# Kernel optimization log

Measured on AMD Instinct MI355X. Metric: run time of the kernel, lower is better.

Reference implementation:

```python
import jax, jax.numpy as jnp
import numpy as np

H = 5  # hidden size
SEQ = 512
BATCH = 16384


def _lstm_layer(x, Wih, Whh, bih, bhh):
    # x: (B, S, D_in); weights follow PyTorch layout: W (4H, D), gate order i,f,g,o
    B = x.shape[0]
    b = bih + bhh
    xs = jnp.swapaxes(x, 0, 1)  # (S, B, D_in)
    # precompute input projections for all timesteps: (S, B, 4H)
    xproj = jnp.einsum('sbd,gd->sbg', xs, Wih) + b

    def step(carry, xp):
        h, c = carry
        gates = xp + h @ Whh.T  # (B, 4H)
        i, f, g, o = jnp.split(gates, 4, axis=-1)
        i = jax.nn.sigmoid(i)
        f = jax.nn.sigmoid(f)
        g = jnp.tanh(g)
        o = jax.nn.sigmoid(o)
        c = f * c + i * g
        h = o * jnp.tanh(c)
        return (h, c), h

    h0 = jnp.zeros((B, H), dtype=x.dtype)
    c0 = jnp.zeros((B, H), dtype=x.dtype)
    _, hs = jax.lax.scan(step, (h0, c0), xproj)  # hs: (S, B, H)
    return jnp.swapaxes(hs, 0, 1)  # (B, S, H)


def setup_inputs() -> dict:
    key = jax.random.key(0)
    ks = jax.random.split(key, 13)
    s = 1.0 / np.sqrt(H)
    u = lambda k, shp: jax.random.uniform(k, shp, jnp.float32, -s, s)
    return {
        'x': jax.random.normal(ks[0], (BATCH, SEQ, 1), jnp.float32),
        'Wih0': u(ks[1], (4 * H, 1)),
        'Whh0': u(ks[2], (4 * H, H)),
        'bih0': u(ks[3], (4 * H,)),
        'bhh0': u(ks[4], (4 * H,)),
        'Wih1': u(ks[5], (4 * H, H)),
        'Whh1': u(ks[6], (4 * H, H)),
        'bih1': u(ks[7], (4 * H,)),
        'bhh1': u(ks[8], (4 * H,)),
        'W1': jax.random.uniform(ks[9], (512, SEQ * H), jnp.float32, -1 / np.sqrt(SEQ * H), 1 / np.sqrt(SEQ * H)),
        'b1': jax.random.uniform(ks[10], (512,), jnp.float32, -1 / np.sqrt(SEQ * H), 1 / np.sqrt(SEQ * H)),
        'W2': jax.random.uniform(ks[11], (1, 512), jnp.float32, -1 / np.sqrt(512), 1 / np.sqrt(512)),
        'b2': jax.random.uniform(ks[12], (1,), jnp.float32, -1 / np.sqrt(512), 1 / np.sqrt(512)),
    }


def reference(x, Wih0, Whh0, bih0, bhh0, Wih1, Whh1, bih1, bhh1, W1, b1, W2, b2):
    h = _lstm_layer(x, Wih0, Whh0, bih0, bhh0)   # (B, S, 5)
    h = _lstm_layer(h, Wih1, Whh1, bih1, bhh1)   # (B, S, 5)
    h = h.reshape(h.shape[0], -1)                # (B, S*5)
    h = h @ W1.T + b1                            # (B, 512)
    out = h @ W2.T + b2                          # (B, 1)
    return out
```

## Files before the change

kernel.cpp:

```cpp
#include <hip/hip_runtime.h>

#define BATCH 16384
#define SEQ 512

typedef float f4 __attribute__((ext_vector_type(4)));
typedef _Float16 half4 __attribute__((ext_vector_type(4)));

#define SIGS (-1.44269504088896f)
#define TNHS (-2.88539008177793f)

union HB2 { unsigned int u[2]; half4 h; };

__device__ __forceinline__ float bpermf(int addr, float v) {
    return __int_as_float(__builtin_amdgcn_ds_bpermute(addr, __float_as_int(v)));
}
__device__ __forceinline__ unsigned int h16(float v) {
    return (unsigned int)__builtin_bit_cast(unsigned short, (_Float16)v);
}
__device__ __forceinline__ unsigned int lolo(unsigned int a, unsigned int b) {
    return __builtin_amdgcn_perm(b, a, 0x05040100u);
}

__device__ __forceinline__ void act3(const f4& dA, const f4& dD, const f4& dC,
                                     float& c0, float& c4, float& c1,
                                     float& hA, float& h4, float& hC) {
    float A0 = __builtin_amdgcn_exp2f(dA[0]), F0 = __builtin_amdgcn_exp2f(dA[1]);
    float B0 = __builtin_amdgcn_exp2f(dA[2]), O0 = __builtin_amdgcn_exp2f(dA[3]);
    float A1 = __builtin_amdgcn_exp2f(dD[0]), F1 = __builtin_amdgcn_exp2f(dD[1]);
    float B1 = __builtin_amdgcn_exp2f(dD[2]), O1 = __builtin_amdgcn_exp2f(dD[3]);
    float A2 = __builtin_amdgcn_exp2f(dC[0]), F2 = __builtin_amdgcn_exp2f(dC[1]);
    float B2 = __builtin_amdgcn_exp2f(dC[2]), O2 = __builtin_amdgcn_exp2f(dC[3]);

    float t0 = 1.0f + A0, t1 = 1.0f + A1, t2 = 1.0f + A2;
    float ab0 = fmaf(t0, B0, t0), ab1 = fmaf(t1, B1, t1), ab2 = fmaf(t2, B2, t2);
    float D0 = fmaf(ab0, F0, ab0), D1 = fmaf(ab1, F1, ab1), D2 = fmaf(ab2, F2, ab2);
    float p01 = D0 * D1, p12 = D1 * D2, p02 = D0 * D2;
    float r = __builtin_amdgcn_rcpf(p01 * D2);
    float r0 = r * p12, r1 = r * p02, r2 = r * p01;

    float bm0 = 1.0f - B0, bm1 = 1.0f - B1, bm2 = 1.0f - B2;
    float w0 = fmaf(bm0, F0, bm0), w1 = fmaf(bm1, F1, bm1), w2 = fmaf(bm2, F2, bm2);
    c0 = fmaf(ab0 * r0, c0, w0 * r0);
    c4 = fmaf(ab1 * r1, c4, w1 * r1);
    c1 = fmaf(ab2 * r2, c1, w2 * r2);

    float pc0 = fminf(c0 * TNHS, 17.0f);
    float pc1 = fminf(c4 * TNHS, 17.0f);
    float pc2 = fminf(c1 * TNHS, 17.0f);
    float Ce0 = __builtin_amdgcn_exp2f(pc0);
    float Ce1 = __builtin_amdgcn_exp2f(pc1);
    float Ce2 = __builtin_amdgcn_exp2f(pc2);
    float o0 = 1.0f + O0, o1 = 1.0f + O1, o2 = 1.0f + O2;
    float e0 = fmaf(o0, Ce0, o0), e1 = fmaf(o1, Ce1, o1), e2 = fmaf(o2, Ce2, o2);
    float q01 = e0 * e1, q12 = e1 * e2, q02 = e0 * e2;
    float rr = __builtin_amdgcn_rcpf(q01 * e2);
    hA = (1.0f - Ce0) * (rr * q12);
    h4 = (1.0f - Ce1) * (rr * q02);
    hC = (1.0f - Ce2) * (rr * q01);
}

__global__ __launch_bounds__(256) void collapse_kernel(
    const float* __restrict__ W1, const float* __restrict__ b1,
    const float* __restrict__ W2, const float* __restrict__ b2,
    float* __restrict__ ws)
{
    const int kl = threadIdx.x & 15;
    const int ms = threadIdx.x >> 4;
    const int k  = blockIdx.x * 16 + kl;
    const float* w1p = W1 + (size_t)(ms * 32) * 2560 + k;
    const float* w2p = W2 + ms * 32;
    float acc = 0.f;
    #pragma unroll 8
    for (int m = 0; m < 32; ++m) acc = fmaf(w2p[m], w1p[(size_t)m * 2560], acc);
    __shared__ float red[16][17];
    red[ms][kl] = acc;
    __syncthreads();
    if (ms == 0) {
        float s = 0.f;
        #pragma unroll
        for (int r = 0; r < 16; ++r) s += red[r][kl];
        const int t = k / 5, u = k % 5;
        if (u < 4) ws[8 * t + 2 * u] = s;
        else { ws[8*t + 1] = s; ws[8*t + 3] = s; ws[8*t + 5] = s; ws[8*t + 7] = s; }
    }
    if (blockIdx.x == 0) {
        const int t = threadIdx.x;
        float p = fmaf(W2[t], b1[t], W2[t + 256] * b1[t + 256]);
        #pragma unroll
        for (int off = 32; off > 0; off >>= 1) p += __shfl_down(p, off);
        __shared__ float cred[4];
        if ((t & 63) == 0) cred[t >> 6] = p;
        __syncthreads();
        if (t == 0) ws[4096] = cred[0] + cred[1] + cred[2] + cred[3] + b2[0];
    }
}

__global__ __launch_bounds__(64)
__attribute__((amdgpu_waves_per_eu(1, 1)))
void lstm_fused_kernel(
    const float* __restrict__ x,
    const float* __restrict__ Wih0, const float* __restrict__ Whh0,
    const float* __restrict__ bih0, const float* __restrict__ bhh0,
    const float* __restrict__ Wih1, const float* __restrict__ Whh1,
    const float* __restrict__ bih1, const float* __restrict__ bhh1,
    const float* __restrict__ ws, float* __restrict__ out)
{
    const int lane = threadIdx.x;
    const int e15  = lane & 15;
    const int g    = lane >> 4;
    const int e    = blockIdx.x * 16 + e15;
    const float sc[4] = {SIGS, SIGS, TNHS, SIGS};

    HB2 aL0a, aL0b, aL1a, aL1b;
    {
        const int m = e15;
        {
            const int u = m >> 2, gi = m & 3, gr = gi * 5 + u;
            const float s = sc[gi];
            float w0 = Whh0[gr * 5 + g];
            float w1 = (g == 0) ? Wih0[gr] : (g == 1 ? Whh0[gr * 5 + 4] : 0.f);
            aL0a.u[0] = h16(w0 * s) | (h16(w1 * s) << 16);
            aL0a.u[1] = 0u;
        }
        {
            float w0 = 0.f, w1 = 0.f, s = 0.f;
            if (m >= 4 && m < 8) {
                const int gi = m - 4, gr = gi * 5 + 4;
                s = sc[gi];
                w0 = Whh0[gr * 5 + g];
                w1 = (g == 0) ? Wih0[gr] : (g == 1 ? Whh0[gr * 5 + 4] : 0.f);
            }
            aL0b.u[0] = h16(w0 * s) | (h16(w1 * s) << 16);
            aL0b.u[1] = 0u;
        }
        {
            const int u = m >> 2, gi = m & 3, gr = gi * 5 + u;
            const float s = sc[gi];
            float w0 = Wih1[gr * 5 + g];
            float w1 = Whh1[gr * 5 + g];
            float w2 = (g == 1) ? Wih1[gr * 5 + 4] : (g == 2 ? Whh1[gr * 5 + 4] : 0.f);
            aL1a.u[0] = h16(w0 * s) | (h16(w1 * s) << 16);
            aL1a.u[1] = h16(w2 * s);
        }
        {
            float w0 = 0.f, w1 = 0.f, w2 = 0.f, s = 0.f;
            if (m >= 8 && m < 12) {
                const int gi = m - 8, gr = gi * 5 + 4;
                s = sc[gi];
                w0 = Wih1[gr * 5 + g];
                w1 = Whh1[gr * 5 + g];
                w2 = (g == 1) ? Wih1[gr * 5 + 4] : (g == 2 ? Whh1[gr * 5 + 4] : 0.f);
            }
            aL1b.u[0] = h16(w0 * s) | (h16(w1 * s) << 16);
            aL1b.u[1] = h16(w2 * s);
        }
    }
    f4 cL0a, cL1a, cb;
    #pragma unroll
    for (int r = 0; r < 4; ++r) {
        cL0a[r] = (bih0[r*5+g] + bhh0[r*5+g]) * sc[r];
        cL1a[r] = (bih1[r*5+g] + bhh1[r*5+g]) * sc[r];
        cb[r]   = (g == 1) ? (bih0[r*5+4] + bhh0[r*5+4]) * sc[r]
                : (g == 2) ? (bih1[r*5+4] + bhh1[r*5+4]) * sc[r] : 0.f;
    }

    const float* xp = x + (size_t)e * SEQ;
    const bool isg0 = (g == 0), isg2 = (g == 2);

    float c0 = 0.f, c1 = 0.f, c4 = 0.f, acc = 0.f, acc4 = 0.f;
    f4 dA, dC, dD;

    {
        unsigned xh0 = h16(xp[0]);
        HB2 b0; b0.u[0] = isg0 ? (xh0 << 16) : 0u; b0.u[1] = 0u;
        dA = __builtin_amdgcn_mfma_f32_16x16x16f16(aL0a.h, b0.h, cL0a, 0, 0, 0);
        f4 dBD = __builtin_amdgcn_mfma_f32_16x16x16f16(aL0b.h, b0.h, cb, 0, 0, 0);
        dC = cL1a;
        dD = dBD;
        float hA, h4, hC;
        act3(dA, dD, dC, c0, c4, c1, hA, h4, hC);
        if (isg2) { h4 = 0.f; c4 = 0.f; }
        hC = 0.f; c1 = 0.f;
        unsigned hx0 = h16(hA) | (h16(h4) << 16);
        unsigned xh1 = h16(xp[1]);
        HB2 B0n, B1n;
        B0n.u[0] = isg0 ? lolo(hx0, xh1) : hx0;  B0n.u[1] = 0u;
        B1n.u[0] = hx0 & 0xFFFFu;                B1n.u[1] = hx0 >> 16;
        dA = __builtin_amdgcn_mfma_f32_16x16x16f16(aL0a.h, B0n.h, cL0a, 0, 0, 0);
        f4 nBD = __builtin_amdgcn_mfma_f32_16x16x16f16(aL0b.h, B0n.h, cb, 0, 0, 0);
        dC = __builtin_amdgcn_mfma_f32_16x16x16f16(aL1a.h, B1n.h, cL1a, 0, 0, 0);
        dD = __builtin_amdgcn_mfma_f32_16x16x16f16(aL1b.h, B1n.h, nBD, 0, 0, 0);
    }

    unsigned xh16[4]; float wM[4], w4b[4];
    #pragma unroll
    for (int u = 0; u < 4; ++u) {
        xh16[u] = h16(xp[2 + u]);
        float2 w = *(const float2*)(ws + 8 * u + 2 * g);
        wM[u] = w.x;  w4b[u] = w.y;
    }

    auto body = [&](unsigned xh_next, float wMu, float w4u) {
        float hA, h4, hC;
        act3(dA, dD, dC, c0, c4, c1, hA, h4, hC);
        acc  = fmaf(hC, wMu, acc);
        acc4 = fmaf(h4, w4u, acc4);
        unsigned hx0  = h16(hA) | (h16(h4) << 16);
        unsigned hc16 = h16(hC);
        HB2 B0n, B1n;
        B0n.u[0] = isg0 ? lolo(hx0, xh_next) : hx0;  B0n.u[1] = 0u;
        B1n.u[0] = lolo(hx0, hc16);                  B1n.u[1] = hx0 >> 16;
        dA = __builtin_amdgcn_mfma_f32_16x16x16f16(aL0a.h, B0n.h, cL0a, 0, 0, 0);
        f4 nBD = __builtin_amdgcn_mfma_f32_16x16x16f16(aL0b.h, B0n.h, cb, 0, 0, 0);
        dC = __builtin_amdgcn_mfma_f32_16x16x16f16(aL1a.h, B1n.h, cL1a, 0, 0, 0);
        dD = __builtin_amdgcn_mfma_f32_16x16x16f16(aL1b.h, B1n.h, nBD, 0, 0, 0);
    };

    for (int m = 1; m < 513; m += 4) {
        unsigned xhn[4]; float wMn[4], w4n[4];
        #pragma unroll
        for (int u = 0; u < 4; ++u) {
            xhn[u] = h16(xp[min(m + 5 + u, SEQ - 1)]);
            const int t = min(m + 3 + u, SEQ - 1);
            float2 w = *(const float2*)(ws + 8 * t + 2 * g);
            wMn[u] = w.x;  w4n[u] = w.y;
        }
        #pragma unroll
        for (int u = 0; u < 4; ++u) body(xh16[u], wM[u], w4b[u]);
        #pragma unroll
        for (int u = 0; u < 4; ++u) { xh16[u] = xhn[u]; wM[u] = wMn[u]; w4b[u] = w4n[u]; }
    }

    float accT = acc + (isg2 ? acc4 : 0.f);
    float t0 = bpermf(e15 << 2, accT);
    float t1 = bpermf((e15 + 16) << 2, accT);
    float t2 = bpermf((e15 + 32) << 2, accT);
    float t3 = bpermf((e15 + 48) << 2, accT);
    if (lane < 16) out[e] = (t0 + t1) + (t2 + t3) + ws[4096];
}

extern "C" void kernel_launch(void* const* d_in, const int* in_sizes, int n_in,
                              void* d_out, int out_size, void* d_ws, size_t ws_size,
                              hipStream_t stream) {
    const float* x    = (const float*)d_in[0];
    const float* Wih0 = (const float*)d_in[1];
    const float* Whh0 = (const float*)d_in[2];
    const float* bih0 = (const float*)d_in[3];
    const float* bhh0 = (const float*)d_in[4];
    const float* Wih1 = (const float*)d_in[5];
    const float* Whh1 = (const float*)d_in[6];
    const float* bih1 = (const float*)d_in[7];
    const float* bhh1 = (const float*)d_in[8];
    const float* W1   = (const float*)d_in[9];
    const float* b1   = (const float*)d_in[10];
    const float* W2   = (const float*)d_in[11];
    const float* b2   = (const float*)d_in[12];
    float* out = (float*)d_out;
    float* ws  = (float*)d_ws;

    collapse_kernel<<<160, 256, 0, stream>>>(W1, b1, W2, b2, ws);
    lstm_fused_kernel<<<BATCH / 16, 64, 0, stream>>>(x, Wih0, Whh0, bih0, bhh0,
                                                     Wih1, Whh1, bih1, bhh1, ws, out);
}
```

Measured before the change: 212.6 us.

## Reorder LSTM step to issue layer-0 MFMAs early and vectorize per-step loads

Inlines the activation code and reorders each step so the layer-0 MFMAs are issued before the layer-1 tail activation (hC) is computed, shortening the recurrent critical path. The collapsed-weight workspace is re-laid out per gate row so four timesteps load as a float4, and x values are loaded in pairs and packed with cvt_pkrtz. Half conversions now use a packed round-toward-zero convert, which changes rounding slightly, and the prologue drops the unused third-unit math. The loop is peeled to avoid clamped indices, at the cost of more code.

After: 206.0 us. -3.1%, faster.

```diff
diff --git a/kernel.cpp b/kernel.cpp
--- a/kernel.cpp
+++ b/kernel.cpp
@@ -17,46 +17,11 @@
 __device__ __forceinline__ unsigned int h16(float v) {
     return (unsigned int)__builtin_bit_cast(unsigned short, (_Float16)v);
 }
+__device__ __forceinline__ unsigned int pk2(float a, float b) {
+    return __builtin_bit_cast(unsigned int, __builtin_amdgcn_cvt_pkrtz(a, b));
+}
 __device__ __forceinline__ unsigned int lolo(unsigned int a, unsigned int b) {
     return __builtin_amdgcn_perm(b, a, 0x05040100u);
-}
-
-__device__ __forceinline__ void act3(const f4& dA, const f4& dD, const f4& dC,
-                                     float& c0, float& c4, float& c1,
-                                     float& hA, float& h4, float& hC) {
-    float A0 = __builtin_amdgcn_exp2f(dA[0]), F0 = __builtin_amdgcn_exp2f(dA[1]);
-    float B0 = __builtin_amdgcn_exp2f(dA[2]), O0 = __builtin_amdgcn_exp2f(dA[3]);
-    float A1 = __builtin_amdgcn_exp2f(dD[0]), F1 = __builtin_amdgcn_exp2f(dD[1]);
-    float B1 = __builtin_amdgcn_exp2f(dD[2]), O1 = __builtin_amdgcn_exp2f(dD[3]);
-    float A2 = __builtin_amdgcn_exp2f(dC[0]), F2 = __builtin_amdgcn_exp2f(dC[1]);
-    float B2 = __builtin_amdgcn_exp2f(dC[2]), O2 = __builtin_amdgcn_exp2f(dC[3]);
-
-    float t0 = 1.0f + A0, t1 = 1.0f + A1, t2 = 1.0f + A2;
-    float ab0 = fmaf(t0, B0, t0), ab1 = fmaf(t1, B1, t1), ab2 = fmaf(t2, B2, t2);
-    float D0 = fmaf(ab0, F0, ab0), D1 = fmaf(ab1, F1, ab1), D2 = fmaf(ab2, F2, ab2);
-    float p01 = D0 * D1, p12 = D1 * D2, p02 = D0 * D2;
-    float r = __builtin_amdgcn_rcpf(p01 * D2);
-    float r0 = r * p12, r1 = r * p02, r2 = r * p01;
-
-    float bm0 = 1.0f - B0, bm1 = 1.0f - B1, bm2 = 1.0f - B2;
-    float w0 = fmaf(bm0, F0, bm0), w1 = fmaf(bm1, F1, bm1), w2 = fmaf(bm2, F2, bm2);
-    c0 = fmaf(ab0 * r0, c0, w0 * r0);
-    c4 = fmaf(ab1 * r1, c4, w1 * r1);
-    c1 = fmaf(ab2 * r2, c1, w2 * r2);
-
-    float pc0 = fminf(c0 * TNHS, 17.0f);
-    float pc1 = fminf(c4 * TNHS, 17.0f);
-    float pc2 = fminf(c1 * TNHS, 17.0f);
-    float Ce0 = __builtin_amdgcn_exp2f(pc0);
-    float Ce1 = __builtin_amdgcn_exp2f(pc1);
-    float Ce2 = __builtin_amdgcn_exp2f(pc2);
-    float o0 = 1.0f + O0, o1 = 1.0f + O1, o2 = 1.0f + O2;
-    float e0 = fmaf(o0, Ce0, o0), e1 = fmaf(o1, Ce1, o1), e2 = fmaf(o2, Ce2, o2);
-    float q01 = e0 * e1, q12 = e1 * e2, q02 = e0 * e2;
-    float rr = __builtin_amdgcn_rcpf(q01 * e2);
-    hA = (1.0f - Ce0) * (rr * q12);
-    h4 = (1.0f - Ce1) * (rr * q02);
-    hC = (1.0f - Ce2) * (rr * q01);
 }
 
 __global__ __launch_bounds__(256) void collapse_kernel(
@@ -80,8 +45,11 @@
         #pragma unroll
         for (int r = 0; r < 16; ++r) s += red[r][kl];
         const int t = k / 5, u = k % 5;
-        if (u < 4) ws[8 * t + 2 * u] = s;
-        else { ws[8*t + 1] = s; ws[8*t + 3] = s; ws[8*t + 5] = s; ws[8*t + 7] = s; }
+        if (u < 4) ws[(u << 10) + 2 * t] = s;
+        else {
+            ws[2*t + 1] = s;        ws[1024 + 2*t + 1] = s;
+            ws[2048 + 2*t + 1] = s; ws[3072 + 2*t + 1] = s;
+        }
     }
     if (blockIdx.x == 0) {
         const int t = threadIdx.x;
@@ -164,71 +132,131 @@
                 : (g == 2) ? (bih1[r*5+4] + bhh1[r*5+4]) * sc[r] : 0.f;
     }
 
-    const float* xp = x + (size_t)e * SEQ;
+    const float* xp  = x + (size_t)e * SEQ;
+    const float* wsg = ws + (g << 10);
     const bool isg0 = (g == 0), isg2 = (g == 2);
+    const unsigned selA = isg0 ? 0x05040100u : 0x03020100u;
+    const unsigned selB = isg0 ? 0x07060100u : 0x03020100u;
 
     float c0 = 0.f, c1 = 0.f, c4 = 0.f, acc = 0.f, acc4 = 0.f;
     f4 dA, dC, dD;
 
     {
-        unsigned xh0 = h16(xp[0]);
+        float2 x01 = *(const float2*)xp;
+        unsigned xh0 = h16(x01.x), xh1 = h16(x01.y);
         HB2 b0; b0.u[0] = isg0 ? (xh0 << 16) : 0u; b0.u[1] = 0u;
         dA = __builtin_amdgcn_mfma_f32_16x16x16f16(aL0a.h, b0.h, cL0a, 0, 0, 0);
         f4 dBD = __builtin_amdgcn_mfma_f32_16x16x16f16(aL0b.h, b0.h, cb, 0, 0, 0);
-        dC = cL1a;
-        dD = dBD;
-        float hA, h4, hC;
-        act3(dA, dD, dC, c0, c4, c1, hA, h4, hC);
+        float A0 = __builtin_amdgcn_exp2f(dA[0]),  F0 = __builtin_amdgcn_exp2f(dA[1]);
+        float B0 = __builtin_amdgcn_exp2f(dA[2]),  O0 = __builtin_amdgcn_exp2f(dA[3]);
+        float A1 = __builtin_amdgcn_exp2f(dBD[0]), F1 = __builtin_amdgcn_exp2f(dBD[1]);
+        float B1 = __builtin_amdgcn_exp2f(dBD[2]), O1 = __builtin_amdgcn_exp2f(dBD[3]);
+        float t0 = 1.f + A0, t1 = 1.f + A1;
+        float ab0 = fmaf(t0, B0, t0), ab1 = fmaf(t1, B1, t1);
+        float D0 = fmaf(ab0, F0, ab0), D1 = fmaf(ab1, F1, ab1);
+        float r = __builtin_amdgcn_rcpf(D0 * D1);
+        float r0 = r * D1, r1 = r * D0;
+        float bm0 = 1.f - B0, bm1 = 1.f - B1;
+        float w0 = fmaf(bm0, F0, bm0), w1 = fmaf(bm1, F1, bm1);
+        c0 = fmaf(ab0 * r0, c0, w0 * r0);
+        c4 = fmaf(ab1 * r1, c4, w1 * r1);
+        float Ce0 = __builtin_amdgcn_exp2f(fminf(c0 * TNHS, 17.f));
+        float Ce1 = __builtin_amdgcn_exp2f(fminf(c4 * TNHS, 17.f));
+        float o0 = 1.f + O0, o1 = 1.f + O1;
+        float e0 = fmaf(o0, Ce0, o0), e1 = fmaf(o1, Ce1, o1);
+        float rr = __builtin_amdgcn_rcpf(e0 * e1);
+        float hA = (1.f - Ce0) * (rr * e1);
+        float h4 = (1.f - Ce1) * (rr * e0);
         if (isg2) { h4 = 0.f; c4 = 0.f; }
-        hC = 0.f; c1 = 0.f;
-        unsigned hx0 = h16(hA) | (h16(h4) << 16);
-        unsigned xh1 = h16(xp[1]);
+        unsigned hx0 = pk2(hA, h4);
         HB2 B0n, B1n;
         B0n.u[0] = isg0 ? lolo(hx0, xh1) : hx0;  B0n.u[1] = 0u;
-        B1n.u[0] = hx0 & 0xFFFFu;                B1n.u[1] = hx0 >> 16;
         dA = __builtin_amdgcn_mfma_f32_16x16x16f16(aL0a.h, B0n.h, cL0a, 0, 0, 0);
         f4 nBD = __builtin_amdgcn_mfma_f32_16x16x16f16(aL0b.h, B0n.h, cb, 0, 0, 0);
+        B1n.u[0] = pk2(hA, 0.f);  B1n.u[1] = pk2(h4, 0.f);
         dC = __builtin_amdgcn_mfma_f32_16x16x16f16(aL1a.h, B1n.h, cL1a, 0, 0, 0);
         dD = __builtin_amdgcn_mfma_f32_16x16x16f16(aL1b.h, B1n.h, nBD, 0, 0, 0);
     }
 
-    unsigned xh16[4]; float wM[4], w4b[4];
-    #pragma unroll
-    for (int u = 0; u < 4; ++u) {
-        xh16[u] = h16(xp[2 + u]);
-        float2 w = *(const float2*)(ws + 8 * u + 2 * g);
-        wM[u] = w.x;  w4b[u] = w.y;
-    }
-
-    auto body = [&](unsigned xh_next, float wMu, float w4u) {
-        float hA, h4, hC;
-        act3(dA, dD, dC, c0, c4, c1, hA, h4, hC);
+    auto body = [&](unsigned xpair, unsigned sel, float wMu, float w4u) {
+        float A0 = __builtin_amdgcn_exp2f(dA[0]), F0 = __builtin_amdgcn_exp2f(dA[1]);
+        float B0 = __builtin_amdgcn_exp2f(dA[2]), O0 = __builtin_amdgcn_exp2f(dA[3]);
+        float A1 = __builtin_amdgcn_exp2f(dD[0]), F1 = __builtin_amdgcn_exp2f(dD[1]);
+        float B1 = __builtin_amdgcn_exp2f(dD[2]), O1 = __builtin_amdgcn_exp2f(dD[3]);
+        float A2 = __builtin_amdgcn_exp2f(dC[0]), F2 = __builtin_amdgcn_exp2f(dC[1]);
+        float B2 = __builtin_amdgcn_exp2f(dC[2]), O2 = __builtin_amdgcn_exp2f(dC[3]);
+        float t0 = 1.f + A0, t1 = 1.f + A1, t2 = 1.f + A2;
+        float ab0 = fmaf(t0, B0, t0), ab1 = fmaf(t1, B1, t1), ab2 = fmaf(t2, B2, t2);
+        float D0 = fmaf(ab0, F0, ab0), D1 = fmaf(ab1, F1, ab1), D2 = fmaf(ab2, F2, ab2);
+        float p01 = D0 * D1, p12 = D1 * D2, p02 = D0 * D2;
+        float r = __builtin_amdgcn_rcpf(p01 * D2);
+        float r0 = r * p12, r1 = r * p02, r2 = r * p01;
+        float bm0 = 1.f - B0, bm1 = 1.f - B1, bm2 = 1.f - B2;
+        float w0 = fmaf(bm0, F0, bm0), w1 = fmaf(bm1, F1, bm1), w2 = fmaf(bm2, F2, bm2);
+        c0 = fmaf(ab0 * r0, c0, w0 * r0);
+        c4 = fmaf(ab1 * r1, c4, w1 * r1);
+        c1 = fmaf(ab2 * r2, c1, w2 * r2);
+        float Ce0 = __builtin_amdgcn_exp2f(fminf(c0 * TNHS, 17.f));
+        float Ce1 = __builtin_amdgcn_exp2f(fminf(c4 * TNHS, 17.f));
+        float o0 = 1.f + O0, o1 = 1.f + O1;
+        float e0 = fmaf(o0, Ce0, o0), e1 = fmaf(o1, Ce1, o1);
+        float rr = __builtin_amdgcn_rcpf(e0 * e1);
+        float hA = (1.f - Ce0) * (rr * e1);
+        float h4 = (1.f - Ce1) * (rr * e0);
+        unsigned hx0 = pk2(hA, h4);
+        HB2 B0n;
+        B0n.u[0] = __builtin_amdgcn_perm(xpair, hx0, sel);  B0n.u[1] = 0u;
+        f4 nA  = __builtin_amdgcn_mfma_f32_16x16x16f16(aL0a.h, B0n.h, cL0a, 0, 0, 0);
+        f4 nBD = __builtin_amdgcn_mfma_f32_16x16x16f16(aL0b.h, B0n.h, cb, 0, 0, 0);
+        float Ce2 = __builtin_amdgcn_exp2f(fminf(c1 * TNHS, 17.f));
+        float o2 = 1.f + O2;
+        float e2 = fmaf(o2, Ce2, o2);
+        float hC = (1.f - Ce2) * __builtin_amdgcn_rcpf(e2);
         acc  = fmaf(hC, wMu, acc);
         acc4 = fmaf(h4, w4u, acc4);
-        unsigned hx0  = h16(hA) | (h16(h4) << 16);
-        unsigned hc16 = h16(hC);
-        HB2 B0n, B1n;
-        B0n.u[0] = isg0 ? lolo(hx0, xh_next) : hx0;  B0n.u[1] = 0u;
-        B1n.u[0] = lolo(hx0, hc16);                  B1n.u[1] = hx0 >> 16;
-        dA = __builtin_amdgcn_mfma_f32_16x16x16f16(aL0a.h, B0n.h, cL0a, 0, 0, 0);
-        f4 nBD = __builtin_amdgcn_mfma_f32_16x16x16f16(aL0b.h, B0n.h, cb, 0, 0, 0);
+        HB2 B1n;
+        B1n.u[0] = pk2(hA, hC);  B1n.u[1] = pk2(h4, 0.f);
         dC = __builtin_amdgcn_mfma_f32_16x16x16f16(aL1a.h, B1n.h, cL1a, 0, 0, 0);
         dD = __builtin_amdgcn_mfma_f32_16x16x16f16(aL1b.h, B1n.h, nBD, 0, 0, 0);
+        dA = nA;
     };
 
-    for (int m = 1; m < 513; m += 4) {
-        unsigned xhn[4]; float wMn[4], w4n[4];
-        #pragma unroll
-        for (int u = 0; u < 4; ++u) {
-            xhn[u] = h16(xp[min(m + 5 + u, SEQ - 1)]);
-            const int t = min(m + 3 + u, SEQ - 1);
-            float2 w = *(const float2*)(ws + 8 * t + 2 * g);
-            wMn[u] = w.x;  w4n[u] = w.y;
-        }
-        #pragma unroll
-        for (int u = 0; u < 4; ++u) body(xh16[u], wM[u], w4b[u]);
-        #pragma unroll
-        for (int u = 0; u < 4; ++u) { xh16[u] = xhn[u]; wM[u] = wMn[u]; w4b[u] = w4n[u]; }
+    unsigned xqa, xqb;  float4 wqa, wqb;
+    {
+        float2 xi0 = *(const float2*)(xp + 2);
+        float2 xi1 = *(const float2*)(xp + 4);
+        xqa = pk2(xi0.x, xi0.y);  xqb = pk2(xi1.x, xi1.y);
+        wqa = *(const float4*)(wsg);
+        wqb = *(const float4*)(wsg + 4);
+    }
+    for (int m = 1; m < 502; m += 4) {
+        float2 xi0 = *(const float2*)(xp + m + 5);
+        float2 xi1 = *(const float2*)(xp + m + 7);
+        unsigned nxa = pk2(xi0.x, xi0.y), nxb = pk2(xi1.x, xi1.y);
+        float4 nwa = *(const float4*)(wsg + 2 * (m + 3));
+        float4 nwb = *(const float4*)(wsg + 2 * (m + 3) + 4);
+        body(xqa, selA, wqa.x, wqa.y);
+        body(xqa, selB, wqa.z, wqa.w);
+        body(xqb, selA, wqb.x, wqb.y);
+        body(xqb, selB, wqb.z, wqb.w);
+        xqa = nxa; xqb = nxb; wqa = nwa; wqb = nwb;
+    }
+    {
+        unsigned nxa = pk2(xp[510], xp[511]);
+        unsigned nxb = pk2(xp[511], xp[511]);
+        float4 nwa = *(const float4*)(wsg + 2 * 508);
+        float4 nwb = *(const float4*)(wsg + 2 * 508 + 4);
+        body(xqa, selA, wqa.x, wqa.y);
+        body(xqa, selB, wqa.z, wqa.w);
+        body(xqb, selA, wqb.x, wqb.y);
+        body(xqb, selB, wqb.z, wqb.w);
+        xqa = nxa; xqb = nxb; wqa = nwa; wqb = nwb;
+    }
+    {
+        body(xqa, selA, wqa.x, wqa.y);
+        body(xqa, selB, wqa.z, wqa.w);
+        body(xqb, selA, wqb.x, wqb.y);
+        body(xqb, selB, wqb.z, wqb.w);
     }
 
     float accT = acc + (isg2 ? acc4 : 0.f);
```
